# Optimization experiments

Measured on AMD Instinct MI355X. Metric: run time of the kernel, lower is better.

The kernel has to match this reference:

```python
import jax, jax.numpy as jnp
import numpy as np

B, D = 8192, 128
TEMP = 0.07
EPS = 1e-12  # F.normalize default eps (clamp on norm)


def _l2norm(x):
    n = jnp.sqrt(jnp.sum(x * x, axis=1, keepdims=True))
    return x / jnp.maximum(n, EPS)


def setup_inputs() -> dict:
    key = jax.random.key(0)
    k1, k2, k3, k4 = jax.random.split(key, 4)
    return {
        "feat_fv": jax.random.normal(k1, (B, D), dtype=jnp.float32),
        "feat_fi": jax.random.normal(k2, (B, D), dtype=jnp.float32),
        "feat_v": jax.random.normal(k3, (B, D), dtype=jnp.float32),
        "feat_i": jax.random.normal(k4, (B, D), dtype=jnp.float32),
    }


def reference(feat_fv, feat_fi, feat_v, feat_i):
    fv = _l2norm(feat_fv)
    fi = _l2norm(feat_fi)
    v = _l2norm(feat_v)
    vi = _l2norm(feat_i)

    # positive logits: per-sample dot products [B]
    pos_v = jnp.sum(fv * v, axis=1)
    pos_i = jnp.sum(fi * vi, axis=1)
    use_v = pos_v >= pos_i                      # branch condition per row
    pos = jnp.where(use_v, pos_v, pos_i)        # [B]

    # full pairwise dot products, branch-select per row
    Sv = jnp.einsum('bd,kd->bk', fv, v)         # [B, B]
    Si = jnp.einsum('bd,kd->bk', fi, vi)        # [B, B]
    S = jnp.where(use_v[:, None], Sv, Si)       # [B, B]

    n = S.shape[0]
    diag = jnp.eye(n, dtype=bool)
    # negatives exclude the positive (diagonal) entry -> mask to -inf
    neg_logits = jnp.where(diag, -jnp.inf, S / TEMP)  # [B, B]

    # cross-entropy with target class 0 (the positive), reduction='none':
    # loss_b = logsumexp([pos/T, negs/T]) - pos/T
    lse = jnp.logaddexp(pos / TEMP, jax.scipy.special.logsumexp(neg_logits, axis=1))
    return lse - pos / TEMP
```

## Files before the change

kernel.cpp:

```cpp
#include <hip/hip_runtime.h>
#include <math.h>

#define Bsz 8192
#define Dd  128
#define BM  64
#define NSLICE 8
#define ROT2(x) ((((x) << 2) | ((x) >> 4)) & 63)

typedef __attribute__((ext_vector_type(8))) short short8;
typedef __attribute__((ext_vector_type(4))) float float4v;

static constexpr float INV_T = 1.0f / 0.07f;

static __device__ inline unsigned pack_bf16(float x, float y) {
    union { float f; unsigned u; } a, b;
    a.f = x; b.f = y;
    unsigned ra = a.u + 0x7FFF + ((a.u >> 16) & 1);
    unsigned rb = b.u + 0x7FFF + ((b.u >> 16) & 1);
    return (ra >> 16) | (rb & 0xFFFF0000u);
}

__global__ void init_kernel(unsigned long long* __restrict__ cnt) {
    if (threadIdx.x == 0) cnt[0] = 0ull;
}

__global__ __launch_bounds__(1024) void prep_kernel(
    const float4* __restrict__ fv4, const float4* __restrict__ fi4,
    const float4* __restrict__ v4,  const float4* __restrict__ vi4,
    unsigned* __restrict__ Xb, uint2* __restrict__ Yf0, uint2* __restrict__ Yf1,
    float* __restrict__ posArr, int* __restrict__ origArr, int* __restrict__ flagArr,
    float* __restrict__ lAcc, unsigned long long* __restrict__ cnt)
{
    __shared__ unsigned sT0[32 * 66];
    __shared__ unsigned sT1[32 * 66];
    __shared__ int sFlagL[32];
    __shared__ int sRank[32];
    __shared__ unsigned sBase[2];

    const int t    = threadIdx.x;
    const int wave = t >> 6;
    const int lane = t & 63;
    const int half = lane >> 5;
    const int c    = lane & 31;
    const int rl   = wave * 2 + half;
    const int b    = blockIdx.x * 32 + rl;
    const int src  = b * 32 + c;

    const float4 afv = fv4[src];
    const float4 afi = fi4[src];
    const float4 av  = v4[src];
    const float4 avi = vi4[src];

    float nfv = afv.x*afv.x + afv.y*afv.y + afv.z*afv.z + afv.w*afv.w;
    float nfi = afi.x*afi.x + afi.y*afi.y + afi.z*afi.z + afi.w*afi.w;
    float nv  = av.x*av.x   + av.y*av.y   + av.z*av.z   + av.w*av.w;
    float nvi = avi.x*avi.x + avi.y*avi.y + avi.z*avi.z + avi.w*avi.w;
    float dv  = afv.x*av.x  + afv.y*av.y  + afv.z*av.z  + afv.w*av.w;
    float di  = afi.x*avi.x + afi.y*avi.y + afi.z*avi.z + afi.w*avi.w;

    #pragma unroll
    for (int m = 1; m < 32; m <<= 1) {
        nfv += __shfl_xor(nfv, m);
        nfi += __shfl_xor(nfi, m);
        nv  += __shfl_xor(nv,  m);
        nvi += __shfl_xor(nvi, m);
        dv  += __shfl_xor(dv,  m);
        di  += __shfl_xor(di,  m);
    }

    const float rnfv = 1.0f / fmaxf(sqrtf(nfv), 1e-12f);
    const float rnfi = 1.0f / fmaxf(sqrtf(nfi), 1e-12f);
    const float rnv  = 1.0f / fmaxf(sqrtf(nv ), 1e-12f);
    const float rnvi = 1.0f / fmaxf(sqrtf(nvi), 1e-12f);

    const float pos_v = dv * rnfv * rnv;
    const float pos_i = di * rnfi * rnvi;
    const bool useV = (pos_v >= pos_i);
    const float pos = useV ? pos_v : pos_i;

    uint2 w0y = make_uint2(pack_bf16(av.x  * rnv,  av.y  * rnv),
                           pack_bf16(av.z  * rnv,  av.w  * rnv));
    uint2 w1y = make_uint2(pack_bf16(avi.x * rnvi, avi.y * rnvi),
                           pack_bf16(avi.z * rnvi, avi.w * rnvi));
    *(uint2*)&sT0[rl * 66 + c * 2] = w0y;
    *(uint2*)&sT1[rl * 66 + c * 2] = w1y;
    if (c == 0) sFlagL[rl] = useV ? 0 : 1;
    __syncthreads();

    if (t < 64) {
        const int f = (lane < 32) ? sFlagL[lane] : 2;
        const unsigned long long m0 = __ballot(f == 0);
        const unsigned long long m1 = __ballot(f == 1);
        if (lane == 0) {
            const unsigned long long add =
                (unsigned long long)__popcll(m0) | ((unsigned long long)__popcll(m1) << 32);
            const unsigned long long ret = atomicAdd(cnt, add);
            sBase[0] = (unsigned)(ret & 0xffffffffull);
            sBase[1] = (unsigned)(ret >> 32);
        }
        if (lane < 32) {
            const unsigned long long below = (1ull << lane) - 1ull;
            sRank[lane] = (f == 0) ? (int)__popcll(m0 & below) : (int)__popcll(m1 & below);
        }
    }

    {
        const int tl = t >> 9;
        const int kc = (t >> 7) & 3;
        const int lp = (t >> 1) & 63;
        const int w0 = (t & 1) * 2;
        const int row = tl * 16 + (lp & 15);
        const int s   = kc * 16 + (lp >> 4) * 4 + w0;
        Yf0[blockIdx.x * 1024 + t] = *(const uint2*)&sT0[row * 66 + s];
        Yf1[blockIdx.x * 1024 + t] = *(const uint2*)&sT1[row * 66 + s];
    }
    __syncthreads();

    const int f  = sFlagL[rl];
    const int rk = sRank[rl];
    const int p  = (f == 0) ? (int)(sBase[0] + rk) : (Bsz - 1 - (int)(sBase[1] + rk));

    const float sc = useV ? rnfv : rnfi;
    ((uint2*)Xb)[p * 32 + c] = make_uint2(pack_bf16(afv.x * sc, afv.y * sc),
                                          pack_bf16(afv.z * sc, afv.w * sc));
    if (!useV)
        ((uint2*)Xb)[p * 32 + c] = make_uint2(pack_bf16(afi.x * sc, afi.y * sc),
                                              pack_bf16(afi.z * sc, afi.w * sc));

    if (c == 0) {
        posArr[p]  = pos;
        origArr[p] = b;
        flagArr[p] = f;
        lAcc[p]    = 0.0f;
    }
}

__global__ __launch_bounds__(256, 4) void main_kernel(
    const unsigned short* __restrict__ Xb,
    const uint4* __restrict__ Yf0q, const uint4* __restrict__ Yf1q,
    const int* __restrict__ flagArr, float* __restrict__ lAcc)
{
    __shared__ uint4 sXf[1024];
    __shared__ int sFlag[BM];
    __shared__ int sHas[2];

    const int t    = threadIdx.x;
    const int wave = t >> 6;
    const int lane = t & 63;
    const int quad = lane >> 4;
    const int mrow = lane & 15;
    const int slice = blockIdx.x & 7;
    const int p0    = (blockIdx.x >> 3) * BM;

    if (t < 2) sHas[t] = 0;
    __syncthreads();
    if (t < BM) {
        const int f = flagArr[p0 + t];
        sFlag[t] = f;
        atomicOr(&sHas[f], 1);
    }

    #pragma unroll
    for (int it = 0; it < 4; ++it) {
        const int i = t + it * 256;
        const int row = i >> 4, ch = i & 15;
        const uint4 val = ((const uint4*)Xb)[(p0 + row) * 16 + ch];
        const int blk16 = (row >> 4) * 4 + (ch >> 2);
        const int slot  = (ch & 3) * 16 + (row & 15);
        sXf[blk16 * 64 + ROT2(slot)] = val;
    }
    __syncthreads();

    short8 afr[4][4];
    #pragma unroll
    for (int rt = 0; rt < 4; ++rt)
        #pragma unroll
        for (int kc = 0; kc < 4; ++kc)
            afr[rt][kc] = *(const short8*)&sXf[(rt * 4 + kc) * 64 + ROT2(lane)];

    unsigned frmask = 0;
    #pragma unroll
    for (int rt = 0; rt < 4; ++rt)
        #pragma unroll
        for (int r = 0; r < 4; ++r)
            frmask |= (unsigned)sFlag[rt * 16 + quad * 4 + r] << (rt * 4 + r);

    float rowsum[4][4] = {};
    const int g0 = slice * 64 + wave * 16;

    for (int phase = 0; phase < 2; ++phase) {
        if (!sHas[phase]) continue;
        const uint4* __restrict__ yb = (phase ? Yf1q : Yf0q) + (size_t)g0 * 256 + lane;

        short8 b0 = *(const short8*)&yb[0];
        short8 b1 = *(const short8*)&yb[64];
        short8 b2 = *(const short8*)&yb[128];
        short8 b3 = *(const short8*)&yb[192];

        #pragma unroll 1
        for (int jt = 0; jt < 16; ++jt) {
            float4v acc[4] = {};
            #pragma unroll
            for (int rt = 0; rt < 4; ++rt)
                acc[rt] = __builtin_amdgcn_mfma_f32_16x16x32_bf16(afr[rt][0], b0, acc[rt], 0, 0, 0);
            #pragma unroll
            for (int rt = 0; rt < 4; ++rt)
                acc[rt] = __builtin_amdgcn_mfma_f32_16x16x32_bf16(afr[rt][1], b1, acc[rt], 0, 0, 0);
            if (jt < 15) {
                b0 = *(const short8*)&yb[256];
                b1 = *(const short8*)&yb[320];
            }
            #pragma unroll
            for (int rt = 0; rt < 4; ++rt)
                acc[rt] = __builtin_amdgcn_mfma_f32_16x16x32_bf16(afr[rt][2], b2, acc[rt], 0, 0, 0);
            #pragma unroll
            for (int rt = 0; rt < 4; ++rt)
                acc[rt] = __builtin_amdgcn_mfma_f32_16x16x32_bf16(afr[rt][3], b3, acc[rt], 0, 0, 0);
            if (jt < 15) {
                b2 = *(const short8*)&yb[384];
                b3 = *(const short8*)&yb[448];
            }
            yb += 256;

            #pragma unroll
            for (int rt = 0; rt < 4; ++rt)
                #pragma unroll
                for (int r = 0; r < 4; ++r)
                    if ((int)((frmask >> (rt * 4 + r)) & 1u) == phase)
                        rowsum[rt][r] += __expf(acc[rt][r] * INV_T - INV_T);
        }
    }

    #pragma unroll
    for (int m = 1; m < 16; m <<= 1)
        #pragma unroll
        for (int rt = 0; rt < 4; ++rt)
            #pragma unroll
            for (int r = 0; r < 4; ++r)
                rowsum[rt][r] += __shfl_xor(rowsum[rt][r], m);

    if (mrow == 0) {
        #pragma unroll
        for (int rt = 0; rt < 4; ++rt)
            #pragma unroll
            for (int r = 0; r < 4; ++r)
                atomicAdd(&lAcc[p0 + rt * 16 + quad * 4 + r], rowsum[rt][r]);
    }
}

__global__ __launch_bounds__(256) void finish_kernel(
    const float* __restrict__ lAcc, const float* __restrict__ posArr,
    const int* __restrict__ origArr, float* __restrict__ out)
{
    const int p = blockIdx.x * 256 + threadIdx.x;
    out[origArr[p]] = logf(lAcc[p]) + INV_T - posArr[p] * INV_T;
}

extern "C" void kernel_launch(void* const* d_in, const int* in_sizes, int n_in,
                              void* d_out, int out_size, void* d_ws, size_t ws_size,
                              hipStream_t stream)
{
    const float4* fv = (const float4*)d_in[0];
    const float4* fi = (const float4*)d_in[1];
    const float4* v  = (const float4*)d_in[2];
    const float4* vi = (const float4*)d_in[3];
    float* out = (float*)d_out;

    unsigned short* Xb  = (unsigned short*)d_ws;
    unsigned short* Yf0 = Xb  + Bsz * Dd;
    unsigned short* Yf1 = Yf0 + Bsz * Dd;
    float* posArr = (float*)(Yf1 + Bsz * Dd);
    float* lAcc   = posArr + Bsz;
    int*  origArr = (int*)(lAcc + Bsz);
    int*  flagArr = origArr + Bsz;
    unsigned long long* cnt = (unsigned long long*)(flagArr + Bsz);

    hipLaunchKernelGGL(init_kernel, dim3(1), dim3(64), 0, stream, cnt);
    hipLaunchKernelGGL(prep_kernel, dim3(Bsz / 32), dim3(1024), 0, stream,
                       fv, fi, v, vi, (unsigned*)Xb, (uint2*)Yf0, (uint2*)Yf1,
                       posArr, origArr, flagArr, lAcc, cnt);
    hipLaunchKernelGGL(main_kernel, dim3((Bsz / BM) * NSLICE), dim3(256), 0, stream,
                       Xb, (const uint4*)Yf0, (const uint4*)Yf1, flagArr, lAcc);
    hipLaunchKernelGGL(finish_kernel, dim3(Bsz / 256), dim3(256), 0, stream,
                       lAcc, posArr, origArr, out);
}
```

Baseline: 106.7 us.

## Fuse finish into main kernel via last-block counter and simplify exp loop

Drops the separate finish kernel. The last of the NSLICE blocks per row block, found with an acq_rel atomic counter, now computes the final log loss, which saves one launch. The inner loop also stops computing exp only for the flag-selected rows. It now accumulates exp2 with a fused multiply-add for every row and filters by flag only at the final atomicAdd. The register double-buffered prefetch of B fragments is replaced by plain loads at the top of each iteration, which may expose load latency.

```diff
diff --git a/kernel.cpp b/kernel.cpp
--- a/kernel.cpp
+++ b/kernel.cpp
@@ -5,12 +5,15 @@
 #define Dd  128
 #define BM  64
 #define NSLICE 8
+#define NRB (Bsz / BM)
 #define ROT2(x) ((((x) << 2) | ((x) >> 4)) & 63)
 
 typedef __attribute__((ext_vector_type(8))) short short8;
 typedef __attribute__((ext_vector_type(4))) float float4v;
 
 static constexpr float INV_T = 1.0f / 0.07f;
+static constexpr float K1 =  20.60992915555662f;
+static constexpr float K2 = -20.60992915555662f;
 
 static __device__ inline unsigned pack_bf16(float x, float y) {
     union { float f; unsigned u; } a, b;
@@ -20,8 +23,11 @@
     return (ra >> 16) | (rb & 0xFFFF0000u);
 }
 
-__global__ void init_kernel(unsigned long long* __restrict__ cnt) {
-    if (threadIdx.x == 0) cnt[0] = 0ull;
+__global__ void init_kernel(unsigned long long* __restrict__ cnt,
+                            int* __restrict__ done) {
+    const int t = threadIdx.x;
+    if (t == 0) cnt[0] = 0ull;
+    if (t < NRB) done[t] = 0;
 }
 
 __global__ __launch_bounds__(1024) void prep_kernel(
@@ -138,11 +144,14 @@
 __global__ __launch_bounds__(256, 4) void main_kernel(
     const unsigned short* __restrict__ Xb,
     const uint4* __restrict__ Yf0q, const uint4* __restrict__ Yf1q,
-    const int* __restrict__ flagArr, float* __restrict__ lAcc)
+    const int* __restrict__ flagArr, float* __restrict__ lAcc,
+    const float* __restrict__ posArr, const int* __restrict__ origArr,
+    int* __restrict__ done, float* __restrict__ out)
 {
     __shared__ uint4 sXf[1024];
     __shared__ int sFlag[BM];
     __shared__ int sHas[2];
+    __shared__ int sLast;
 
     const int t    = threadIdx.x;
     const int wave = t >> 6;
@@ -150,7 +159,8 @@
     const int quad = lane >> 4;
     const int mrow = lane & 15;
     const int slice = blockIdx.x & 7;
-    const int p0    = (blockIdx.x >> 3) * BM;
+    const int rb    = blockIdx.x >> 3;
+    const int p0    = rb * BM;
 
     if (t < 2) sHas[t] = 0;
     __syncthreads();
@@ -178,27 +188,21 @@
         for (int kc = 0; kc < 4; ++kc)
             afr[rt][kc] = *(const short8*)&sXf[(rt * 4 + kc) * 64 + ROT2(lane)];
 
-    unsigned frmask = 0;
-    #pragma unroll
-    for (int rt = 0; rt < 4; ++rt)
-        #pragma unroll
-        for (int r = 0; r < 4; ++r)
-            frmask |= (unsigned)sFlag[rt * 16 + quad * 4 + r] << (rt * 4 + r);
-
-    float rowsum[4][4] = {};
     const int g0 = slice * 64 + wave * 16;
 
     for (int phase = 0; phase < 2; ++phase) {
         if (!sHas[phase]) continue;
         const uint4* __restrict__ yb = (phase ? Yf1q : Yf0q) + (size_t)g0 * 256 + lane;
 
-        short8 b0 = *(const short8*)&yb[0];
-        short8 b1 = *(const short8*)&yb[64];
-        short8 b2 = *(const short8*)&yb[128];
-        short8 b3 = *(const short8*)&yb[192];
+        float rowsum[4][4] = {};
 
         #pragma unroll 1
         for (int jt = 0; jt < 16; ++jt) {
+            const short8 b0 = *(const short8*)&yb[0];
+            const short8 b1 = *(const short8*)&yb[64];
+            const short8 b2 = *(const short8*)&yb[128];
+            const short8 b3 = *(const short8*)&yb[192];
+
             float4v acc[4] = {};
             #pragma unroll
             for (int rt = 0; rt < 4; ++rt)
@@ -206,54 +210,54 @@
             #pragma unroll
             for (int rt = 0; rt < 4; ++rt)
                 acc[rt] = __builtin_amdgcn_mfma_f32_16x16x32_bf16(afr[rt][1], b1, acc[rt], 0, 0, 0);
-            if (jt < 15) {
-                b0 = *(const short8*)&yb[256];
-                b1 = *(const short8*)&yb[320];
-            }
             #pragma unroll
             for (int rt = 0; rt < 4; ++rt)
                 acc[rt] = __builtin_amdgcn_mfma_f32_16x16x32_bf16(afr[rt][2], b2, acc[rt], 0, 0, 0);
             #pragma unroll
             for (int rt = 0; rt < 4; ++rt)
                 acc[rt] = __builtin_amdgcn_mfma_f32_16x16x32_bf16(afr[rt][3], b3, acc[rt], 0, 0, 0);
-            if (jt < 15) {
-                b2 = *(const short8*)&yb[384];
-                b3 = *(const short8*)&yb[448];
-            }
-            yb += 256;
 
             #pragma unroll
             for (int rt = 0; rt < 4; ++rt)
                 #pragma unroll
                 for (int r = 0; r < 4; ++r)
-                    if ((int)((frmask >> (rt * 4 + r)) & 1u) == phase)
-                        rowsum[rt][r] += __expf(acc[rt][r] * INV_T - INV_T);
-        }
-    }
-
-    #pragma unroll
-    for (int m = 1; m < 16; m <<= 1)
+                    rowsum[rt][r] += exp2f(fmaf(acc[rt][r], K1, K2));
+
+            yb += 256;
+        }
+
         #pragma unroll
-        for (int rt = 0; rt < 4; ++rt)
-            #pragma unroll
-            for (int r = 0; r < 4; ++r)
-                rowsum[rt][r] += __shfl_xor(rowsum[rt][r], m);
-
-    if (mrow == 0) {
-        #pragma unroll
-        for (int rt = 0; rt < 4; ++rt)
-            #pragma unroll
-            for (int r = 0; r < 4; ++r)
-                atomicAdd(&lAcc[p0 + rt * 16 + quad * 4 + r], rowsum[rt][r]);
-    }
-}
-
-__global__ __launch_bounds__(256) void finish_kernel(
-    const float* __restrict__ lAcc, const float* __restrict__ posArr,
-    const int* __restrict__ origArr, float* __restrict__ out)
-{
-    const int p = blockIdx.x * 256 + threadIdx.x;
-    out[origArr[p]] = logf(lAcc[p]) + INV_T - posArr[p] * INV_T;
+        for (int m = 1; m < 16; m <<= 1)
+            #pragma unroll
+            for (int rt = 0; rt < 4; ++rt)
+                #pragma unroll
+                for (int r = 0; r < 4; ++r)
+                    rowsum[rt][r] += __shfl_xor(rowsum[rt][r], m);
+
+        if (mrow == 0) {
+            #pragma unroll
+            for (int rt = 0; rt < 4; ++rt)
+                #pragma unroll
+                for (int r = 0; r < 4; ++r) {
+                    const int row = rt * 16 + quad * 4 + r;
+                    if (sFlag[row] == phase)
+                        atomicAdd(&lAcc[p0 + row], rowsum[rt][r]);
+                }
+        }
+    }
+
+    __threadfence();
+    __syncthreads();
+    if (t == 0)
+        sLast = (__hip_atomic_fetch_add(&done[rb], 1, __ATOMIC_ACQ_REL,
+                                        __HIP_MEMORY_SCOPE_AGENT) == NSLICE - 1);
+    __syncthreads();
+    if (sLast && t < BM) {
+        const int p = p0 + t;
+        const float a = __hip_atomic_load(&lAcc[p], __ATOMIC_RELAXED,
+                                          __HIP_MEMORY_SCOPE_AGENT);
+        out[origArr[p]] = logf(a) + INV_T - posArr[p] * INV_T;
+    }
 }
 
 extern "C" void kernel_launch(void* const* d_in, const int* in_sizes, int n_in,
@@ -273,14 +277,14 @@
     float* lAcc   = posArr + Bsz;
     int*  origArr = (int*)(lAcc + Bsz);
     int*  flagArr = origArr + Bsz;
-    unsigned long long* cnt = (unsigned long long*)(flagArr + Bsz);
-
-    hipLaunchKernelGGL(init_kernel, dim3(1), dim3(64), 0, stream, cnt);
+    int*  done    = flagArr + Bsz;
+    unsigned long long* cnt = (unsigned long long*)(done + NRB);
+
+    hipLaunchKernelGGL(init_kernel, dim3(1), dim3(128), 0, stream, cnt, done);
     hipLaunchKernelGGL(prep_kernel, dim3(Bsz / 32), dim3(1024), 0, stream,
                        fv, fi, v, vi, (unsigned*)Xb, (uint2*)Yf0, (uint2*)Yf1,
                        posArr, origArr, flagArr, lAcc, cnt);
-    hipLaunchKernelGGL(main_kernel, dim3((Bsz / BM) * NSLICE), dim3(256), 0, stream,
-                       Xb, (const uint4*)Yf0, (const uint4*)Yf1, flagArr, lAcc);
-    hipLaunchKernelGGL(finish_kernel, dim3(Bsz / 256), dim3(256), 0, stream,
-                       lAcc, posArr, origArr, out);
-}
+    hipLaunchKernelGGL(main_kernel, dim3(NRB * NSLICE), dim3(256), 0, stream,
+                       Xb, (const uint4*)Yf0, (const uint4*)Yf1, flagArr, lAcc,
+                       posArr, origArr, done, out);
+}
```

Measured after the change: 186.3 us. +74.6%, slower.
